# Kernel tuning notes

Hardware: AMD Instinct MI355X
Metric: run time of the kernel (lower is better)

## Reference

```python
import jax, jax.numpy as jnp
import numpy as np

N = 50000
E = 800000
IN, HID, OUT = 256, 64, 64
H1, H2 = 4, 1
SLOPE = 0.2  # DGL GATConv default negative_slope


def setup_inputs() -> dict:
    key = jax.random.key(0)
    ks = jax.random.split(key, 12)
    inp = {
        "features": jax.random.normal(ks[0], (N, IN), jnp.float32),
        "src": jax.random.randint(ks[1], (E,), 0, N),
        "dst": jax.random.randint(ks[2], (E,), 0, N),
        # layer 1 params (fc has no bias in DGL; separate bias added post-aggregation)
        "W1": jax.random.normal(ks[3], (IN, H1 * HID), jnp.float32) * (1.0 / np.sqrt(IN)),
        "al1": jax.random.normal(ks[4], (H1, HID), jnp.float32) * 0.1,
        "ar1": jax.random.normal(ks[5], (H1, HID), jnp.float32) * 0.1,
        "b1": jnp.zeros((H1 * HID,), jnp.float32),
        # layer 2 params
        "W2": jax.random.normal(ks[6], (H1 * HID, H2 * OUT), jnp.float32) * (1.0 / np.sqrt(H1 * HID)),
        "al2": jax.random.normal(ks[7], (H2, OUT), jnp.float32) * 0.1,
        "ar2": jax.random.normal(ks[8], (H2, OUT), jnp.float32) * 0.1,
        "b2": jnp.zeros((H2 * OUT,), jnp.float32),
    }
    return inp


def _gat_layer(x, src, dst, W, al, ar, b, H, D):
    # fc projection + reshape to [N, H, D]
    h = (x @ W).reshape(-1, H, D)
    el = jnp.einsum("nhd,hd->nh", h, al)  # [N,H]
    er = jnp.einsum("nhd,hd->nh", h, ar)
    e = jax.nn.leaky_relu(el[src] + er[dst], SLOPE)  # [E,H]
    # segment (per-dst-node) softmax over incoming edges
    emax = jax.ops.segment_max(e, dst, num_segments=N)
    ex = jnp.exp(e - emax[dst])
    denom = jax.ops.segment_sum(ex, dst, num_segments=N)
    a = ex / denom[dst]  # [E,H]
    # weighted gather-scatter aggregation
    out = jax.ops.segment_sum(a[:, :, None] * h[src], dst, num_segments=N)  # [N,H,D]
    return out + b.reshape(1, H, D)


def reference(features, src, dst, W1, al1, ar1, b1, W2, al2, ar2, b2):
    # layer 1: GATConv + elu activation, then flatten heads
    h = _gat_layer(features, src, dst, W1, al1, ar1, b1, H1, HID)
    h = jax.nn.elu(h).reshape(N, H1 * HID)
    # layer 2: GATConv (no activation), then mean over heads
    h = _gat_layer(h, src, dst, W2, al2, ar2, b2, H2, OUT)
    return h.mean(axis=1)  # [N, OUT]
```

## Files before the change

kernel.cpp:

```cpp
#include <hip/hip_runtime.h>
#include <hip/hip_bf16.h>
#include <hip/hip_fp16.h>
#include <math.h>

#define SLOPE 0.2f

typedef __attribute__((ext_vector_type(8))) short bf16x8;
typedef __attribute__((ext_vector_type(4))) float f32x4;

__device__ inline unsigned short f2bf(float f) {
    unsigned u = __float_as_uint(f);
    u += 0x7FFF + ((u >> 16) & 1);
    return (unsigned short)(u >> 16);
}
__device__ inline float bf2f(unsigned short s) {
    return __uint_as_float(((unsigned)s) << 16);
}


__global__ void deg_kernel(const int* __restrict__ dst, int* __restrict__ deg,
                           int* __restrict__ rank, int E) {
    int i = blockIdx.x * blockDim.x + threadIdx.x;
    if (i < E) rank[i] = atomicAdd(&deg[dst[i]], 1);
}

__global__ __launch_bounds__(256) void psum_kernel(const int* __restrict__ deg,
                                                   int* __restrict__ bsum, int n) {
    const int t = threadIdx.x;
    const int i = blockIdx.x * 256 + t;
    int v = (i < n) ? deg[i] : 0;
#pragma unroll
    for (int o = 1; o < 64; o <<= 1) v += __shfl_xor(v, o, 64);
    __shared__ int ws[4];
    if ((t & 63) == 0) ws[t >> 6] = v;
    __syncthreads();
    if (t == 0) bsum[blockIdx.x] = ws[0] + ws[1] + ws[2] + ws[3];
}

__global__ __launch_bounds__(256) void scan2_kernel(const int* __restrict__ deg,
                                                    const int* __restrict__ bsum,
                                                    int* __restrict__ offs, int n) {
    const int b = blockIdx.x, t = threadIdx.x;
    const int lane = t & 63, w = t >> 6;

    int contrib = (t < b) ? bsum[t] : 0;
#pragma unroll
    for (int o = 1; o < 64; o <<= 1) contrib += __shfl_xor(contrib, o, 64);
    __shared__ int wsum[4];
    if (lane == 0) wsum[w] = contrib;
    __syncthreads();
    const int base = wsum[0] + wsum[1] + wsum[2] + wsum[3];

    const int i = b * 256 + t;
    const int v = (i < n) ? deg[i] : 0;
    int incl = v;
#pragma unroll
    for (int o = 1; o < 64; o <<= 1) {
        const int u = __shfl_up(incl, o, 64);
        if (lane >= o) incl += u;
    }
    __shared__ int wtot[4];
    if (lane == 63) wtot[w] = incl;
    __syncthreads();
    int wbase = 0;
#pragma unroll
    for (int k = 0; k < 4; ++k)
        if (k < w) wbase += wtot[k];

    const int excl = base + wbase + incl - v;
    if (i < n) offs[i] = excl;
    if (i == n - 1) offs[n] = excl + v;
}

__global__ void fill_kernel(const int* __restrict__ src, const int* __restrict__ dst,
                            const int* __restrict__ offs, const int* __restrict__ rank,
                            int* __restrict__ csr_src, int E) {
    int i = blockIdx.x * blockDim.x + threadIdx.x;
    if (i < E) {
        csr_src[offs[dst[i]] + rank[i]] = src[i];
    }
}


__global__ void cvt_wt_kernel(const float* __restrict__ W, unsigned short* __restrict__ Wt,
                              int K, int M) {
    const int k = blockIdx.x, c = threadIdx.x;
    Wt[c * K + k] = f2bf(W[k * M + c]);
}

__global__ __launch_bounds__(256) void gemm1_mfma(const float* __restrict__ Xf,
                                                  const unsigned short* __restrict__ Wt,
                                                  const float* __restrict__ AL,
                                                  const float* __restrict__ AR,
                                                  unsigned short* __restrict__ Hout,
                                                  float* __restrict__ el,
                                                  float* __restrict__ er, int n) {
    constexpr int LDR = 72;
    __shared__ __align__(16) unsigned short Xs[128 * LDR];
    __shared__ __align__(16) unsigned short Ws[128 * LDR];

    const int tid = threadIdx.x;
    const int wave = tid >> 6, lane = tid & 63;
    const int col16 = lane & 15, quad = lane >> 4;
    const int node0 = blockIdx.x * 128;
    const int fb = blockIdx.y;

    f32x4 acc[8][2];
#pragma unroll
    for (int ft = 0; ft < 8; ++ft)
#pragma unroll
        for (int nt = 0; nt < 2; ++nt) acc[ft][nt] = (f32x4){0.f, 0.f, 0.f, 0.f};

    const int rr = tid >> 3;
    const int cc = (tid & 7) * 8;

    for (int k0 = 0; k0 < 256; k0 += 64) {
#pragma unroll
        for (int p = 0; p < 4; ++p) {
            const int row = rr + p * 32;
            int gx = node0 + row; if (gx >= n) gx = n - 1;
            const float4* xp = (const float4*)&Xf[(long long)gx * 256 + k0 + cc];
            const float4 a = xp[0];
            const float4 b = xp[1];
            bf16x8 v;
            v[0] = (short)f2bf(a.x); v[1] = (short)f2bf(a.y);
            v[2] = (short)f2bf(a.z); v[3] = (short)f2bf(a.w);
            v[4] = (short)f2bf(b.x); v[5] = (short)f2bf(b.y);
            v[6] = (short)f2bf(b.z); v[7] = (short)f2bf(b.w);
            *(bf16x8*)&Xs[row * LDR + cc] = v;
            *(bf16x8*)&Ws[row * LDR + cc] =
                *(const bf16x8*)&Wt[((long long)(fb * 128 + row)) * 256 + k0 + cc];
        }
        __syncthreads();
#pragma unroll
        for (int ks = 0; ks < 64; ks += 32) {
            bf16x8 bfrag[2];
#pragma unroll
            for (int nt = 0; nt < 2; ++nt)
                bfrag[nt] = *(const bf16x8*)&Xs[(wave * 32 + nt * 16 + col16) * LDR +
                                                ks + quad * 8];
#pragma unroll
            for (int ft = 0; ft < 8; ++ft) {
                const bf16x8 afrag =
                    *(const bf16x8*)&Ws[(ft * 16 + col16) * LDR + ks + quad * 8];
                acc[ft][0] = __builtin_amdgcn_mfma_f32_16x16x32_bf16(afrag, bfrag[0],
                                                                     acc[ft][0], 0, 0, 0);
                acc[ft][1] = __builtin_amdgcn_mfma_f32_16x16x32_bf16(afrag, bfrag[1],
                                                                     acc[ft][1], 0, 0, 0);
            }
        }
        __syncthreads();
    }

    float elp[2][2] = {{0.f, 0.f}, {0.f, 0.f}};
    float erp[2][2] = {{0.f, 0.f}, {0.f, 0.f}};
#pragma unroll
    for (int ft = 0; ft < 8; ++ft) {
        const int hb = ft >> 2;
        const int head = fb * 2 + hb;
        float alw[4], arw[4];
#pragma unroll
        for (int r = 0; r < 4; ++r) {
            const int d = (ft & 3) * 16 + quad * 4 + r;
            alw[r] = AL[head * 64 + d];
            arw[r] = AR[head * 64 + d];
        }
#pragma unroll
        for (int nt = 0; nt < 2; ++nt) {
            const int node = node0 + wave * 32 + nt * 16 + col16;
            if (node < n) {
                ushort4 pk;
                pk.x = f2bf(acc[ft][nt][0]); pk.y = f2bf(acc[ft][nt][1]);
                pk.z = f2bf(acc[ft][nt][2]); pk.w = f2bf(acc[ft][nt][3]);
                *(ushort4*)&Hout[(long long)node * 256 + fb * 128 + ft * 16 + quad * 4] = pk;
            }
#pragma unroll
            for (int r = 0; r < 4; ++r) {
                elp[nt][hb] = fmaf(acc[ft][nt][r], alw[r], elp[nt][hb]);
                erp[nt][hb] = fmaf(acc[ft][nt][r], arw[r], erp[nt][hb]);
            }
        }
    }
#pragma unroll
    for (int nt = 0; nt < 2; ++nt)
#pragma unroll
        for (int hb = 0; hb < 2; ++hb) {
            elp[nt][hb] += __shfl_xor(elp[nt][hb], 16, 64);
            elp[nt][hb] += __shfl_xor(elp[nt][hb], 32, 64);
            erp[nt][hb] += __shfl_xor(erp[nt][hb], 16, 64);
            erp[nt][hb] += __shfl_xor(erp[nt][hb], 32, 64);
        }
    if (quad == 0) {
#pragma unroll
        for (int nt = 0; nt < 2; ++nt) {
            const int node = node0 + wave * 32 + nt * 16 + col16;
            if (node < n) {
#pragma unroll
                for (int hb = 0; hb < 2; ++hb) {
                    el[node * 4 + fb * 2 + hb] = elp[nt][hb];
                    er[node * 4 + fb * 2 + hb] = erp[nt][hb];
                }
            }
        }
    }
}

__global__ __launch_bounds__(256) void gemm2_mfma(const unsigned short* __restrict__ Xbf,
                                                  const unsigned short* __restrict__ Wt,
                                                  const float* __restrict__ AL,
                                                  const float* __restrict__ AR,
                                                  unsigned short* __restrict__ Hout,
                                                  float* __restrict__ el,
                                                  float* __restrict__ er, int n) {
    constexpr int LDR = 72;
    __shared__ __align__(16) unsigned short Xs[128 * LDR];
    __shared__ __align__(16) unsigned short Ws[64 * LDR];

    const int tid = threadIdx.x;
    const int wave = tid >> 6, lane = tid & 63;
    const int col16 = lane & 15, quad = lane >> 4;
    const int node0 = blockIdx.x * 128;

    f32x4 acc[4][2];
#pragma unroll
    for (int ft = 0; ft < 4; ++ft)
#pragma unroll
        for (int nt = 0; nt < 2; ++nt) acc[ft][nt] = (f32x4){0.f, 0.f, 0.f, 0.f};

    const int rr = tid >> 3;
    const int cc = (tid & 7) * 8;

    for (int k0 = 0; k0 < 256; k0 += 64) {
#pragma unroll
        for (int p = 0; p < 4; ++p) {
            const int row = rr + p * 32;
            int gx = node0 + row; if (gx >= n) gx = n - 1;
            *(bf16x8*)&Xs[row * LDR + cc] =
                *(const bf16x8*)&Xbf[(long long)gx * 256 + k0 + cc];
        }
#pragma unroll
        for (int p = 0; p < 2; ++p) {
            const int row = rr + p * 32;
            *(bf16x8*)&Ws[row * LDR + cc] =
                *(const bf16x8*)&Wt[(long long)row * 256 + k0 + cc];
        }
        __syncthreads();
#pragma unroll
        for (int ks = 0; ks < 64; ks += 32) {
            bf16x8 bfrag[2];
#pragma unroll
            for (int nt = 0; nt < 2; ++nt)
                bfrag[nt] = *(const bf16x8*)&Xs[(wave * 32 + nt * 16 + col16) * LDR +
                                                ks + quad * 8];
#pragma unroll
            for (int ft = 0; ft < 4; ++ft) {
                const bf16x8 afrag =
                    *(const bf16x8*)&Ws[(ft * 16 + col16) * LDR + ks + quad * 8];
                acc[ft][0] = __builtin_amdgcn_mfma_f32_16x16x32_bf16(afrag, bfrag[0],
                                                                     acc[ft][0], 0, 0, 0);
                acc[ft][1] = __builtin_amdgcn_mfma_f32_16x16x32_bf16(afrag, bfrag[1],
                                                                     acc[ft][1], 0, 0, 0);
            }
        }
        __syncthreads();
    }

    float elp[2] = {0.f, 0.f}, erp[2] = {0.f, 0.f};
#pragma unroll
    for (int ft = 0; ft < 4; ++ft) {
        float alw[4], arw[4];
#pragma unroll
        for (int r = 0; r < 4; ++r) {
            const int d = ft * 16 + quad * 4 + r;
            alw[r] = AL[d];
            arw[r] = AR[d];
        }
#pragma unroll
        for (int nt = 0; nt < 2; ++nt) {
            const int node = node0 + wave * 32 + nt * 16 + col16;
            if (node < n) {
                ushort4 pk;
                pk.x = __half_as_ushort(__float2half(acc[ft][nt][0]));
                pk.y = __half_as_ushort(__float2half(acc[ft][nt][1]));
                pk.z = __half_as_ushort(__float2half(acc[ft][nt][2]));
                pk.w = __half_as_ushort(__float2half(acc[ft][nt][3]));
                *(ushort4*)&Hout[(long long)node * 64 + ft * 16 + quad * 4] = pk;
            }
#pragma unroll
            for (int r = 0; r < 4; ++r) {
                elp[nt] = fmaf(acc[ft][nt][r], alw[r], elp[nt]);
                erp[nt] = fmaf(acc[ft][nt][r], arw[r], erp[nt]);
            }
        }
    }
#pragma unroll
    for (int nt = 0; nt < 2; ++nt) {
        elp[nt] += __shfl_xor(elp[nt], 16, 64);
        elp[nt] += __shfl_xor(elp[nt], 32, 64);
        erp[nt] += __shfl_xor(erp[nt], 16, 64);
        erp[nt] += __shfl_xor(erp[nt], 32, 64);
    }
    if (quad == 0) {
#pragma unroll
        for (int nt = 0; nt < 2; ++nt) {
            const int node = node0 + wave * 32 + nt * 16 + col16;
            if (node < n) {
                el[node] = elp[nt];
                er[node] = erp[nt];
            }
        }
    }
}

__global__ __launch_bounds__(256) void aggr1_kernel(const unsigned short* __restrict__ Hf,
                                                    const float* __restrict__ el,
                                                    const float* __restrict__ er,
                                                    const int* __restrict__ offs,
                                                    const int* __restrict__ csr,
                                                    const float* __restrict__ bias,
                                                    unsigned short* __restrict__ out,
                                                    int n) {
    const int node = (blockIdx.x * blockDim.x + threadIdx.x) >> 6;
    if (node >= n) return;
    const int lane = threadIdx.x & 63;
    const int g = lane >> 4;
    const int r = lane & 15;
    const int h = r >> 2;
    const int beg = offs[node], end = offs[node + 1];
    const float erv = er[node * 4 + h];

    float acc[16];
#pragma unroll
    for (int q = 0; q < 16; ++q) acc[q] = 0.f;
    float l = 0.f;

    const int nb = (end - beg + 3) >> 2;
#pragma unroll 2
    for (int it = 0; it < nb; ++it) {
        const int ei = beg + it * 4 + g;
        const bool ok = ei < end;
        const int ci = ok ? ei : (end - 1);
        const int s = csr[ci];
        float e = el[s * 4 + h] + erv;
        e = (e > 0.f) ? e : SLOPE * e;
        float p = __expf(fminf(e, 80.f));
        if (!ok) p = 0.f;
        const uint4* hp = (const uint4*)(Hf + (s << 8) + (r << 4));
        const uint4 u0 = hp[0];
        const uint4 u1 = hp[1];
        l += p;
        const unsigned uu[8] = {u0.x, u0.y, u0.z, u0.w, u1.x, u1.y, u1.z, u1.w};
#pragma unroll
        for (int q = 0; q < 8; ++q) {
            const float flo = __uint_as_float(uu[q] << 16);
            const float fhi = __uint_as_float(uu[q] & 0xFFFF0000u);
            acc[2 * q]     = fmaf(p, flo, acc[2 * q]);
            acc[2 * q + 1] = fmaf(p, fhi, acc[2 * q + 1]);
        }
    }

#pragma unroll
    for (int q = 0; q < 16; ++q) {
        acc[q] += __shfl_xor(acc[q], 16, 64);
        acc[q] += __shfl_xor(acc[q], 32, 64);
    }
    l += __shfl_xor(l, 16, 64);
    l += __shfl_xor(l, 32, 64);

    if (g == 0) {
        const float inv = (l > 0.f) ? 1.f / l : 0.f;
        unsigned o[8];
#pragma unroll
        for (int q = 0; q < 8; ++q) {
            float v0 = acc[2 * q]     * inv + bias[r * 16 + 2 * q];
            float v1 = acc[2 * q + 1] * inv + bias[r * 16 + 2 * q + 1];
            v0 = (v0 > 0.f) ? v0 : expm1f(v0);
            v1 = (v1 > 0.f) ? v1 : expm1f(v1);
            o[q] = (unsigned)f2bf(v0) | ((unsigned)f2bf(v1) << 16);
        }
        uint4* op = (uint4*)(out + (node << 8) + (r << 4));
        op[0] = make_uint4(o[0], o[1], o[2], o[3]);
        op[1] = make_uint4(o[4], o[5], o[6], o[7]);
    }
}

__global__ __launch_bounds__(256) void aggr2_kernel(const unsigned short* __restrict__ Hf,
                                                    const float* __restrict__ el,
                                                    const float* __restrict__ er,
                                                    const int* __restrict__ offs,
                                                    const int* __restrict__ csr,
                                                    const float* __restrict__ bias,
                                                    float* __restrict__ out, int n) {
    const int node = (blockIdx.x * blockDim.x + threadIdx.x) >> 6;
    if (node >= n) return;
    const int lane = threadIdx.x & 63;
    const int g = lane >> 4;
    const int r = lane & 15;
    const int beg = offs[node], end = offs[node + 1];
    const float erv = er[node];

    float a0 = 0.f, a1 = 0.f, a2 = 0.f, a3 = 0.f, l = 0.f;
    const int nb = (end - beg + 3) >> 2;
#pragma unroll 2
    for (int it = 0; it < nb; ++it) {
        const int ei = beg + it * 4 + g;
        const bool ok = ei < end;
        const int ci = ok ? ei : (end - 1);
        const int s = csr[ci];
        float e = el[s] + erv;
        e = (e > 0.f) ? e : SLOPE * e;
        float p = __expf(fminf(e, 80.f));
        if (!ok) p = 0.f;
        const uint2 u = *(const uint2*)(Hf + (s << 6) + (r << 2));
        const float h0 = __half2float(__ushort_as_half((unsigned short)(u.x & 0xFFFFu)));
        const float h1 = __half2float(__ushort_as_half((unsigned short)(u.x >> 16)));
        const float h2 = __half2float(__ushort_as_half((unsigned short)(u.y & 0xFFFFu)));
        const float h3 = __half2float(__ushort_as_half((unsigned short)(u.y >> 16)));
        l += p;
        a0 = fmaf(p, h0, a0);
        a1 = fmaf(p, h1, a1);
        a2 = fmaf(p, h2, a2);
        a3 = fmaf(p, h3, a3);
    }

    a0 += __shfl_xor(a0, 16, 64); a0 += __shfl_xor(a0, 32, 64);
    a1 += __shfl_xor(a1, 16, 64); a1 += __shfl_xor(a1, 32, 64);
    a2 += __shfl_xor(a2, 16, 64); a2 += __shfl_xor(a2, 32, 64);
    a3 += __shfl_xor(a3, 16, 64); a3 += __shfl_xor(a3, 32, 64);
    l  += __shfl_xor(l, 16, 64);  l  += __shfl_xor(l, 32, 64);

    if (g == 0) {
        const float inv = (l > 0.f) ? 1.f / l : 0.f;
        const float4 b4 = *(const float4*)(bias + r * 4);
        *(float4*)(out + (node << 6) + (r << 2)) =
            make_float4(fmaf(a0, inv, b4.x), fmaf(a1, inv, b4.y),
                        fmaf(a2, inv, b4.z), fmaf(a3, inv, b4.w));
    }
}


extern "C" void kernel_launch(void* const* d_in, const int* in_sizes, int n_in,
                              void* d_out, int out_size, void* d_ws, size_t ws_size,
                              hipStream_t stream) {
    const float* feat = (const float*)d_in[0];
    const int*   src  = (const int*)d_in[1];
    const int*   dst  = (const int*)d_in[2];
    const float* W1   = (const float*)d_in[3];
    const float* al1  = (const float*)d_in[4];
    const float* ar1  = (const float*)d_in[5];
    const float* b1   = (const float*)d_in[6];
    const float* W2   = (const float*)d_in[7];
    const float* al2  = (const float*)d_in[8];
    const float* ar2  = (const float*)d_in[9];
    const float* b2   = (const float*)d_in[10];
    float* out = (float*)d_out;

    const int IN = 256, HID = 64, OUT = 64, H1 = 4, H2 = 1;
    const int N = in_sizes[0] / IN;
    const int E = in_sizes[1];

    size_t off = 0;
    auto alloc = [&](size_t bytes) {
        void* p = (char*)d_ws + off;
        off += (bytes + 255) & ~(size_t)255;
        return p;
    };
    int*   deg    = (int*)alloc((size_t)N * 4);
    int*   offs   = (int*)alloc((size_t)(N + 1) * 4);
    int*   bsum   = (int*)alloc((size_t)256 * 4);
    int*   rank   = (int*)alloc((size_t)E * 4);
    int*   csr    = (int*)alloc((size_t)E * 4);
    unsigned short* h1   = (unsigned short*)alloc((size_t)N * H1 * HID * 2);
    unsigned short* wt1  = (unsigned short*)alloc((size_t)IN * H1 * HID * 2);
    unsigned short* wt2  = (unsigned short*)alloc((size_t)H1 * HID * H2 * OUT * 2);
    unsigned short* x2bf = (unsigned short*)alloc((size_t)N * H1 * HID * 2);
    unsigned short* h2   = (unsigned short*)alloc((size_t)N * H2 * OUT * 2);
    float* el1    = (float*)alloc((size_t)N * H1 * 4);
    float* er1    = (float*)alloc((size_t)N * H1 * 4);
    float* el2    = (float*)alloc((size_t)N * H2 * 4);
    float* er2    = (float*)alloc((size_t)N * H2 * 4);
    (void)ws_size;

    hipMemsetAsync(deg, 0, (size_t)N * 4, stream);

    const int nb = (N + 255) / 256;
    deg_kernel<<<(E + 255) / 256, 256, 0, stream>>>(dst, deg, rank, E);
    psum_kernel<<<nb, 256, 0, stream>>>(deg, bsum, N);
    scan2_kernel<<<nb, 256, 0, stream>>>(deg, bsum, offs, N);
    fill_kernel<<<(E + 255) / 256, 256, 0, stream>>>(src, dst, offs, rank, csr, E);

    cvt_wt_kernel<<<256, 256, 0, stream>>>(W1, wt1, 256, 256);
    cvt_wt_kernel<<<256, 64, 0, stream>>>(W2, wt2, 256, 64);

    {
        dim3 g((N + 127) / 128, 2);
        gemm1_mfma<<<g, 256, 0, stream>>>(feat, wt1, al1, ar1, h1, el1, er1, N);
    }
    aggr1_kernel<<<(N + 3) / 4, 256, 0, stream>>>(h1, el1, er1, offs, csr, b1, x2bf, N);
    gemm2_mfma<<<(N + 127) / 128, 256, 0, stream>>>(x2bf, wt2, al2, ar2, h2, el2, er2, N);
    aggr2_kernel<<<(N + 3) / 4, 256, 0, stream>>>(h2, el2, er2, offs, csr, b2, out, N);
}
```

Baseline: 302.1 us.

## Fuse CSR construction into cooperative kernel, merge weight casts, prefetch csr indices

Replaces the memset, degree, partial-sum, scan and fill kernels with one cooperative grid-synchronized kernel that builds the CSR. The two weight-conversion launches are merged into one. Both aggregation loops now software-prefetch the next neighbor index so its load overlaps the current edge's gather. This is meant to cut launch and inter-kernel gaps, at the cost of five grid-wide barriers and a dependence on every block being co-resident.

```diff
diff --git a/kernel.cpp b/kernel.cpp
--- a/kernel.cpp
+++ b/kernel.cpp
@@ -1,7 +1,10 @@
 #include <hip/hip_runtime.h>
+#include <hip/hip_cooperative_groups.h>
 #include <hip/hip_bf16.h>
 #include <hip/hip_fp16.h>
 #include <math.h>
+
+namespace cg = cooperative_groups;
 
 #define SLOPE 0.2f
 
@@ -17,75 +20,105 @@
     return __uint_as_float(((unsigned)s) << 16);
 }
 
-
-__global__ void deg_kernel(const int* __restrict__ dst, int* __restrict__ deg,
-                           int* __restrict__ rank, int E) {
-    int i = blockIdx.x * blockDim.x + threadIdx.x;
-    if (i < E) rank[i] = atomicAdd(&deg[dst[i]], 1);
-}
-
-__global__ __launch_bounds__(256) void psum_kernel(const int* __restrict__ deg,
-                                                   int* __restrict__ bsum, int n) {
+__global__ __launch_bounds__(256) void csr_coop(const int* __restrict__ src,
+                                                const int* __restrict__ dst,
+                                                int* __restrict__ deg,
+                                                int* __restrict__ rank,
+                                                int* __restrict__ offs,
+                                                int* __restrict__ bsum,
+                                                int* __restrict__ csr, int n, int E) {
+    cg::grid_group grid = cg::this_grid();
     const int t = threadIdx.x;
-    const int i = blockIdx.x * 256 + t;
-    int v = (i < n) ? deg[i] : 0;
-#pragma unroll
-    for (int o = 1; o < 64; o <<= 1) v += __shfl_xor(v, o, 64);
+    const int b = blockIdx.x;
+    const int G = gridDim.x;
+    const int tid = b * blockDim.x + t;
+    const int nthr = G * blockDim.x;
+    const int lane = t & 63, w = t >> 6;
+    const int C = (n + G - 1) / G;
+
+    for (int i = tid; i < n; i += nthr) deg[i] = 0;
+    grid.sync();
+
+    for (int i = tid; i < E; i += nthr) rank[i] = atomicAdd(&deg[dst[i]], 1);
+    grid.sync();
+
     __shared__ int ws[4];
-    if ((t & 63) == 0) ws[t >> 6] = v;
-    __syncthreads();
-    if (t == 0) bsum[blockIdx.x] = ws[0] + ws[1] + ws[2] + ws[3];
-}
-
-__global__ __launch_bounds__(256) void scan2_kernel(const int* __restrict__ deg,
-                                                    const int* __restrict__ bsum,
-                                                    int* __restrict__ offs, int n) {
-    const int b = blockIdx.x, t = threadIdx.x;
-    const int lane = t & 63, w = t >> 6;
-
-    int contrib = (t < b) ? bsum[t] : 0;
-#pragma unroll
-    for (int o = 1; o < 64; o <<= 1) contrib += __shfl_xor(contrib, o, 64);
-    __shared__ int wsum[4];
-    if (lane == 0) wsum[w] = contrib;
-    __syncthreads();
-    const int base = wsum[0] + wsum[1] + wsum[2] + wsum[3];
-
-    const int i = b * 256 + t;
-    const int v = (i < n) ? deg[i] : 0;
-    int incl = v;
-#pragma unroll
-    for (int o = 1; o < 64; o <<= 1) {
-        const int u = __shfl_up(incl, o, 64);
-        if (lane >= o) incl += u;
-    }
-    __shared__ int wtot[4];
-    if (lane == 63) wtot[w] = incl;
-    __syncthreads();
-    int wbase = 0;
-#pragma unroll
-    for (int k = 0; k < 4; ++k)
-        if (k < w) wbase += wtot[k];
-
-    const int excl = base + wbase + incl - v;
-    if (i < n) offs[i] = excl;
-    if (i == n - 1) offs[n] = excl + v;
-}
-
-__global__ void fill_kernel(const int* __restrict__ src, const int* __restrict__ dst,
-                            const int* __restrict__ offs, const int* __restrict__ rank,
-                            int* __restrict__ csr_src, int E) {
-    int i = blockIdx.x * blockDim.x + threadIdx.x;
-    if (i < E) {
-        csr_src[offs[dst[i]] + rank[i]] = src[i];
-    }
-}
-
-
-__global__ void cvt_wt_kernel(const float* __restrict__ W, unsigned short* __restrict__ Wt,
-                              int K, int M) {
+    {
+        const int i = b * C + t;
+        int v = (t < C && i < n) ? deg[i] : 0;
+#pragma unroll
+        for (int o = 1; o < 64; o <<= 1) v += __shfl_xor(v, o, 64);
+        if (lane == 0) ws[w] = v;
+        __syncthreads();
+        if (t == 0) bsum[b] = ws[0] + ws[1] + ws[2] + ws[3];
+    }
+    grid.sync();
+
+    if (b == 0) {
+        int loc[4];
+        int tsum = 0;
+#pragma unroll
+        for (int q = 0; q < 4; ++q) {
+            const int j = t * 4 + q;
+            loc[q] = (j < G) ? bsum[j] : 0;
+            tsum += loc[q];
+        }
+        int incl = tsum;
+#pragma unroll
+        for (int o = 1; o < 64; o <<= 1) {
+            const int u = __shfl_up(incl, o, 64);
+            if (lane >= o) incl += u;
+        }
+        __shared__ int wtot[4];
+        if (lane == 63) wtot[w] = incl;
+        __syncthreads();
+        int wbase = 0;
+#pragma unroll
+        for (int k = 0; k < 4; ++k)
+            if (k < w) wbase += wtot[k];
+        int run = wbase + incl - tsum;
+#pragma unroll
+        for (int q = 0; q < 4; ++q) {
+            const int j = t * 4 + q;
+            if (j < G) { bsum[j] = run; run += loc[q]; }
+        }
+    }
+    grid.sync();
+
+    {
+        const int i = b * C + t;
+        const int v = (t < C && i < n) ? deg[i] : 0;
+        int incl = v;
+#pragma unroll
+        for (int o = 1; o < 64; o <<= 1) {
+            const int u = __shfl_up(incl, o, 64);
+            if (lane >= o) incl += u;
+        }
+        __shared__ int wtot2[4];
+        if (lane == 63) wtot2[w] = incl;
+        __syncthreads();
+        int wbase = 0;
+#pragma unroll
+        for (int k = 0; k < 4; ++k)
+            if (k < w) wbase += wtot2[k];
+        const int excl = bsum[b] + wbase + incl - v;
+        if (t < C && i < n) {
+            offs[i] = excl;
+            if (i == n - 1) offs[n] = excl + v;
+        }
+    }
+    grid.sync();
+
+    for (int i = tid; i < E; i += nthr)
+        csr[offs[dst[i]] + rank[i]] = src[i];
+}
+
+__global__ void cvt_w_kernel(const float* __restrict__ W1, const float* __restrict__ W2,
+                             unsigned short* __restrict__ Wt1,
+                             unsigned short* __restrict__ Wt2) {
     const int k = blockIdx.x, c = threadIdx.x;
-    Wt[c * K + k] = f2bf(W[k * M + c]);
+    Wt1[c * 256 + k] = f2bf(W1[k * 256 + c]);
+    if (c < 64) Wt2[c * 256 + k] = f2bf(W2[k * 64 + c]);
 }
 
 __global__ __launch_bounds__(256) void gemm1_mfma(const float* __restrict__ Xf,
@@ -335,12 +368,14 @@
     float l = 0.f;
 
     const int nb = (end - beg + 3) >> 2;
+    int ci = beg + g; if (ci >= end) ci = end - 1;
+    int s = csr[ci];
 #pragma unroll 2
     for (int it = 0; it < nb; ++it) {
         const int ei = beg + it * 4 + g;
         const bool ok = ei < end;
-        const int ci = ok ? ei : (end - 1);
-        const int s = csr[ci];
+        int nci = ei + 4; if (nci >= end) nci = end - 1;
+        const int sn = csr[nci];
         float e = el[s * 4 + h] + erv;
         e = (e > 0.f) ? e : SLOPE * e;
         float p = __expf(fminf(e, 80.f));
@@ -357,6 +392,7 @@
             acc[2 * q]     = fmaf(p, flo, acc[2 * q]);
             acc[2 * q + 1] = fmaf(p, fhi, acc[2 * q + 1]);
         }
+        s = sn;
     }
 
 #pragma unroll
@@ -401,12 +437,14 @@
 
     float a0 = 0.f, a1 = 0.f, a2 = 0.f, a3 = 0.f, l = 0.f;
     const int nb = (end - beg + 3) >> 2;
+    int ci = beg + g; if (ci >= end) ci = end - 1;
+    int s = csr[ci];
 #pragma unroll 2
     for (int it = 0; it < nb; ++it) {
         const int ei = beg + it * 4 + g;
         const bool ok = ei < end;
-        const int ci = ok ? ei : (end - 1);
-        const int s = csr[ci];
+        int nci = ei + 4; if (nci >= end) nci = end - 1;
+        const int sn = csr[nci];
         float e = el[s] + erv;
         e = (e > 0.f) ? e : SLOPE * e;
         float p = __expf(fminf(e, 80.f));
@@ -421,6 +459,7 @@
         a1 = fmaf(p, h1, a1);
         a2 = fmaf(p, h2, a2);
         a3 = fmaf(p, h3, a3);
+        s = sn;
     }
 
     a0 += __shfl_xor(a0, 16, 64); a0 += __shfl_xor(a0, 32, 64);
@@ -467,7 +506,7 @@
     };
     int*   deg    = (int*)alloc((size_t)N * 4);
     int*   offs   = (int*)alloc((size_t)(N + 1) * 4);
-    int*   bsum   = (int*)alloc((size_t)256 * 4);
+    int*   bsum   = (int*)alloc((size_t)1024 * 4);
     int*   rank   = (int*)alloc((size_t)E * 4);
     int*   csr    = (int*)alloc((size_t)E * 4);
     unsigned short* h1   = (unsigned short*)alloc((size_t)N * H1 * HID * 2);
@@ -481,16 +520,18 @@
     float* er2    = (float*)alloc((size_t)N * H2 * 4);
     (void)ws_size;
 
-    hipMemsetAsync(deg, 0, (size_t)N * 4, stream);
-
-    const int nb = (N + 255) / 256;
-    deg_kernel<<<(E + 255) / 256, 256, 0, stream>>>(dst, deg, rank, E);
-    psum_kernel<<<nb, 256, 0, stream>>>(deg, bsum, N);
-    scan2_kernel<<<nb, 256, 0, stream>>>(deg, bsum, offs, N);
-    fill_kernel<<<(E + 255) / 256, 256, 0, stream>>>(src, dst, offs, rank, csr, E);
-
-    cvt_wt_kernel<<<256, 256, 0, stream>>>(W1, wt1, 256, 256);
-    cvt_wt_kernel<<<256, 64, 0, stream>>>(W2, wt2, 256, 64);
+    {
+        const int*  srcp = src;
+        const int*  dstp = dst;
+        int* degp = deg; int* rankp = rank; int* offsp = offs;
+        int* bsump = bsum; int* csrp = csr;
+        int  Nv = N, Ev = E;
+        void* args[] = {&srcp, &dstp, &degp, &rankp, &offsp, &bsump, &csrp, &Nv, &Ev};
+        hipLaunchCooperativeKernel((void*)csr_coop, dim3(1024), dim3(256),
+                                   args, 0, stream);
+    }
+
+    cvt_w_kernel<<<256, 256, 0, stream>>>(W1, W2, wt1, wt2);
 
     {
         dim3 g((N + 127) / 128, 2);
```

New measurement: 779.3 us. 158% more time.
